# Optimization experiments

Measured on AMD Instinct MI355X. Metric: run time of the kernel, lower is better.

## Reference

```python
import jax, jax.numpy as jnp
import numpy as np

N_NODES = 20000
NUM_KERNELS = 2
K_DIFF = 10  # max_diffusion_step
IN_DIM = 128
HID = 128
COMB = IN_DIM + HID  # 256
N_EDGES = 640000


def setup_inputs() -> dict:
    key = jax.random.key(0)
    ks = jax.random.split(key, 6)
    inp = jax.random.normal(ks[0], (N_NODES, IN_DIM), dtype=jnp.float32)
    hidden = jax.random.normal(ks[1], (N_NODES, HID), dtype=jnp.float32)
    edge_index = jax.random.randint(ks[2], (NUM_KERNELS, 2, N_EDGES), 0, N_NODES, dtype=jnp.int32)
    # ~row-stochastic-ish weights (avg degree 32) to keep diffusion stable
    edge_weight = jax.random.uniform(ks[3], (NUM_KERNELS, N_EDGES), dtype=jnp.float32) * (1.0 / 32.0)
    num_matrices = NUM_KERNELS * K_DIFF + 1  # 21
    W = jax.random.normal(ks[4], (num_matrices * COMB, HID), dtype=jnp.float32) * (1.0 / np.sqrt(num_matrices * COMB))
    b = jnp.zeros((HID,), dtype=jnp.float32)
    return {"input": inp, "hidden": hidden, "edge_index": edge_index,
            "edge_weight": edge_weight, "W": W, "b": b}


def _gconv(x, edge_index, edge_weight, W, b):
    # x: (N, F). Diffusion (Chebyshev) over each sparse support, concat, project.
    n = x.shape[0]
    feats = [x]  # x_0 shared across kernels
    for k in range(NUM_KERNELS):
        src = edge_index[k, 0]
        dst = edge_index[k, 1]
        w = edge_weight[k][:, None]

        def spmm(v):  # (A v)[dst] = sum_e w_e * v[src_e]
            return jax.ops.segment_sum(v[src] * w, dst, num_segments=n)

        x0, x1 = x, spmm(x)
        feats.append(x1)
        for _ in range(2, K_DIFF + 1):
            x2 = 2.0 * spmm(x1) - x0
            feats.append(x2)
            x0, x1 = x1, x2
    h = jnp.concatenate(feats, axis=1)  # (N, (NUM_KERNELS*K+1)*F)
    return h @ W + b


def reference(input, hidden, edge_index, edge_weight, W, b):
    combined = jnp.concatenate([input, hidden], axis=1)  # (N, COMB)
    r = jax.nn.sigmoid(_gconv(combined, edge_index, edge_weight, W, b))
    u = jax.nn.sigmoid(_gconv(combined, edge_index, edge_weight, W, b))
    combined2 = jnp.concatenate([input, r * hidden], axis=1)
    C = jax.nn.sigmoid(_gconv(combined2, edge_index, edge_weight, W, b))  # activation=sigmoid (default)
    output = u * hidden + (1.0 - u) * C
    return output  # output == new hidden
```

## Files before the change

kernel.cpp:

```cpp
#include <hip/hip_runtime.h>

#define NN 20000
#define NK 2
#define FC 256
#define FH 128
#define NE 640000
#define NB 21

typedef short v8s __attribute__((ext_vector_type(8)));
typedef float v4f __attribute__((ext_vector_type(4)));

__device__ __forceinline__ float bf2f(unsigned short h) {
    union { unsigned int u; float f; } v; v.u = ((unsigned int)h) << 16; return v.f;
}
__device__ __forceinline__ unsigned short f2bf(float f) {
    union { float f; unsigned int u; } v; v.f = f;
    unsigned int r = v.u + 0x7FFF + ((v.u >> 16) & 1);
    return (unsigned short)(r >> 16);
}
__device__ __forceinline__ float bflo(unsigned int v) {
    union { unsigned int u; float f; } t; t.u = v << 16; return t.f;
}
__device__ __forceinline__ float bfhi(unsigned int v) {
    union { unsigned int u; float f; } t; t.u = v & 0xffff0000u; return t.f;
}


__global__ __launch_bounds__(256) void k_hist(const int* __restrict__ ei, int* __restrict__ cnt) {
    int i = blockIdx.x * 256 + threadIdx.x;
    int k = i / NE, e = i - k * NE;
    int dst = ei[(size_t)k * 2 * NE + NE + e];
    atomicAdd(&cnt[k * NN + dst], 1);
}

__global__ __launch_bounds__(1024) void k_scan(const int* __restrict__ cnt, int* __restrict__ rp) {
    int k = blockIdx.x;
    __shared__ int part[1024];
    int t = threadIdx.x;
    int loc[20];
    int s = 0;
    if (t < 1000) {
#pragma unroll
        for (int j = 0; j < 20; ++j) { loc[j] = cnt[k * NN + t * 20 + j]; s += loc[j]; }
    }
    part[t] = s;
    __syncthreads();
    for (int off = 1; off < 1024; off <<= 1) {
        int add = (t >= off) ? part[t - off] : 0;
        __syncthreads();
        part[t] += add;
        __syncthreads();
    }
    int excl = (t == 0) ? 0 : part[t - 1];
    if (t < 1000) {
        int run = excl;
#pragma unroll
        for (int j = 0; j < 20; ++j) { rp[k * (NN + 1) + t * 20 + j] = run; run += loc[j]; }
        if (t == 999) rp[k * (NN + 1) + NN] = run;
    }
}

__global__ __launch_bounds__(256) void k_fill(const int* __restrict__ ei, const float* __restrict__ ew,
                                              const int* __restrict__ rp, int* __restrict__ fcnt,
                                              int2* __restrict__ ep) {
    int i = blockIdx.x * 256 + threadIdx.x;
    int k = i / NE, e = i - k * NE;
    int src = ei[(size_t)k * 2 * NE + e];
    int dst = ei[(size_t)k * 2 * NE + NE + e];
    int pos = rp[k * (NN + 1) + dst] + atomicAdd(&fcnt[k * NN + dst], 1);
    int2 pk; pk.x = src; pk.y = __float_as_int(ew[(size_t)k * NE + e]);
    ep[(size_t)k * NE + pos] = pk;
}


__global__ __launch_bounds__(256) void k_comb(const float* __restrict__ in, const float* __restrict__ hid,
                                              unsigned short* __restrict__ comb) {
    int i = blockIdx.x * 256 + threadIdx.x;
    int r = i >> 6, c4 = i & 63;
    float4 v = (c4 < 32) ? ((const float4*)(in  + (size_t)r * FH))[c4]
                         : ((const float4*)(hid + (size_t)r * FH))[c4 - 32];
    ushort4 o; o.x = f2bf(v.x); o.y = f2bf(v.y); o.z = f2bf(v.z); o.w = f2bf(v.w);
    *(ushort4*)&comb[(size_t)r * FC + c4 * 4] = o;
}


__global__ __launch_bounds__(256) void k_wcvt(const float* __restrict__ W, unsigned short* __restrict__ Wt) {
    int i = blockIdx.x * 256 + threadIdx.x;
    int blk = i >> 15;
    int rem = i & 32767;
    int n = rem >> 8, kk = rem & 255;
    Wt[i] = f2bf(W[((size_t)blk * FC + kk) * FH + n]);
}


#define LDK 72

__global__ __launch_bounds__(256, 2) void k_gemm(const unsigned short* __restrict__ X,
        const unsigned short* __restrict__ Wt, unsigned short* __restrict__ outb,
        float* __restrict__ outf, int jstep) {
    __shared__ unsigned short Xs[64 * LDK];
    __shared__ unsigned short Ws[128 * LDK];
    int t = threadIdx.x;
    int w = t >> 6, l = t & 63;
    int l15 = l & 15, lg = l >> 4;
    int bm = blockIdx.x * 64;
    int blk = jstep + 10 * blockIdx.y;
    const unsigned short* Wb = Wt + (size_t)blk * FH * FC;
    v4f acc[4][2];
#pragma unroll
    for (int a = 0; a < 4; ++a)
#pragma unroll
        for (int b = 0; b < 2; ++b) acc[a][b] = (v4f){0.f, 0.f, 0.f, 0.f};

    for (int c = 0; c < 4; ++c) {
#pragma unroll
        for (int i = 0; i < 2; ++i) {
            int s = t + i * 256;
            int row = s >> 3, c8 = s & 7;
            int grow = bm + row; if (grow >= NN) grow = NN - 1;
            *(v8s*)&Xs[row * LDK + c8 * 8] = *(const v8s*)(X + (size_t)grow * FC + c * 64 + c8 * 8);
        }
#pragma unroll
        for (int i = 0; i < 4; ++i) {
            int s = t + i * 256;
            int n = s >> 3, k8 = s & 7;
            *(v8s*)&Ws[n * LDK + k8 * 8] = *(const v8s*)(Wb + (size_t)n * FC + c * 64 + k8 * 8);
        }
        __syncthreads();
#pragma unroll
        for (int ks2 = 0; ks2 < 2; ++ks2) {
            int ko = ks2 * 32 + lg * 8;
            v8s a[4], b[2];
#pragma unroll
            for (int mf = 0; mf < 4; ++mf) a[mf] = *(const v8s*)&Xs[(mf * 16 + l15) * LDK + ko];
#pragma unroll
            for (int nf = 0; nf < 2; ++nf) b[nf] = *(const v8s*)&Ws[(w * 32 + nf * 16 + l15) * LDK + ko];
#pragma unroll
            for (int mf = 0; mf < 4; ++mf)
#pragma unroll
                for (int nf = 0; nf < 2; ++nf)
                    acc[mf][nf] = __builtin_amdgcn_mfma_f32_16x16x32_bf16(a[mf], b[nf], acc[mf][nf], 0, 0, 0);
        }
        __syncthreads();
    }
    unsigned short* ob = outb ? outb + (size_t)blockIdx.y * NN * FH : (unsigned short*)0;
#pragma unroll
    for (int mf = 0; mf < 4; ++mf) {
        int grow0 = bm + mf * 16 + lg * 4;
#pragma unroll
        for (int nf = 0; nf < 2; ++nf) {
            int gcol = w * 32 + nf * 16 + l15;
#pragma unroll
            for (int r = 0; r < 4; ++r) {
                int grow = grow0 + r;
                if (grow < NN) {
                    if (outf) outf[(size_t)grow * FH + gcol] = acc[mf][nf][r];
                    else      ob[(size_t)grow * FH + gcol] = f2bf(acc[mf][nf][r]);
                }
            }
        }
    }
}


__global__ __launch_bounds__(256) void k_spmm(const int* __restrict__ rp, const int2* __restrict__ ep,
        const unsigned short* __restrict__ b1, const unsigned short* __restrict__ b2,
        const unsigned short* __restrict__ y, unsigned short* __restrict__ outp, int mode) {
    int wg = blockIdx.x;
    int xcd = wg & 7, slot = wg >> 3;
    int k = (xcd >= 4) ? 1 : 0;
    int unit = (xcd & 3) * 1250 + slot;
    int lane = threadIdx.x & 63;
    int row = unit * 4 + (threadIdx.x >> 6);
    int beg = rp[k * (NN + 1) + row], end = rp[k * (NN + 1) + row + 1];
    const unsigned int* b1u = (const unsigned int*)b1 + (size_t)k * NN * 64;
    const long long* epk = (const long long*)(ep + (size_t)k * NE);

    float ax0 = 0.f, ax1 = 0.f, ax2 = 0.f, ax3 = 0.f;
    float ay0 = 0.f, ay1 = 0.f, ay2 = 0.f, ay3 = 0.f;

    for (int e0 = beg; e0 < end; e0 += 64) {
        int idx = e0 + lane;
        long long mye = (idx < end) ? __builtin_nontemporal_load(epk + idx) : 0ll;
        int mx = (int)mye;
        int my = (int)(mye >> 32);
        int cnt = min(64, end - e0);
        int j = 0;
        for (; j + 8 <= cnt; j += 8) {
            int   s0 = __builtin_amdgcn_readlane(mx, j + 0);
            int   s1 = __builtin_amdgcn_readlane(mx, j + 1);
            int   s2 = __builtin_amdgcn_readlane(mx, j + 2);
            int   s3 = __builtin_amdgcn_readlane(mx, j + 3);
            int   s4 = __builtin_amdgcn_readlane(mx, j + 4);
            int   s5 = __builtin_amdgcn_readlane(mx, j + 5);
            int   s6 = __builtin_amdgcn_readlane(mx, j + 6);
            int   s7 = __builtin_amdgcn_readlane(mx, j + 7);
            unsigned int v0 = b1u[(size_t)s0 * 64 + lane];
            unsigned int v1 = b1u[(size_t)s1 * 64 + lane];
            unsigned int v2 = b1u[(size_t)s2 * 64 + lane];
            unsigned int v3 = b1u[(size_t)s3 * 64 + lane];
            unsigned int v4 = b1u[(size_t)s4 * 64 + lane];
            unsigned int v5 = b1u[(size_t)s5 * 64 + lane];
            unsigned int v6 = b1u[(size_t)s6 * 64 + lane];
            unsigned int v7 = b1u[(size_t)s7 * 64 + lane];
            float w0 = __int_as_float(__builtin_amdgcn_readlane(my, j + 0));
            float w1 = __int_as_float(__builtin_amdgcn_readlane(my, j + 1));
            float w2 = __int_as_float(__builtin_amdgcn_readlane(my, j + 2));
            float w3 = __int_as_float(__builtin_amdgcn_readlane(my, j + 3));
            float w4 = __int_as_float(__builtin_amdgcn_readlane(my, j + 4));
            float w5 = __int_as_float(__builtin_amdgcn_readlane(my, j + 5));
            float w6 = __int_as_float(__builtin_amdgcn_readlane(my, j + 6));
            float w7 = __int_as_float(__builtin_amdgcn_readlane(my, j + 7));
            ax0 += w0 * bflo(v0); ay0 += w0 * bfhi(v0);
            ax1 += w1 * bflo(v1); ay1 += w1 * bfhi(v1);
            ax2 += w2 * bflo(v2); ay2 += w2 * bfhi(v2);
            ax3 += w3 * bflo(v3); ay3 += w3 * bfhi(v3);
            ax0 += w4 * bflo(v4); ay0 += w4 * bfhi(v4);
            ax1 += w5 * bflo(v5); ay1 += w5 * bfhi(v5);
            ax2 += w6 * bflo(v6); ay2 += w6 * bfhi(v6);
            ax3 += w7 * bflo(v7); ay3 += w7 * bfhi(v7);
        }
        for (; j < cnt; ++j) {
            int   s = __builtin_amdgcn_readlane(mx, j);
            float w = __int_as_float(__builtin_amdgcn_readlane(my, j));
            unsigned int v = b1u[(size_t)s * 64 + lane];
            ax0 += w * bflo(v); ay0 += w * bfhi(v);
        }
    }
    float ax = (ax0 + ax1) + (ax2 + ax3);
    float ay = (ay0 + ay1) + (ay2 + ay3);

    size_t o = (size_t)(k * NN + row) * 64 + lane;
    float rx, ry;
    if (mode == 0) {
        unsigned int yv = __builtin_nontemporal_load((const unsigned int*)y + o);
        rx = bflo(yv) + 2.f * ax;
        ry = bfhi(yv) + 2.f * ay;
    } else if (mode == 1) {
        unsigned int yv = __builtin_nontemporal_load((const unsigned int*)y + o);
        unsigned int bv = __builtin_nontemporal_load((const unsigned int*)b2 + o);
        rx = bflo(yv) + 2.f * ax - bflo(bv);
        ry = bfhi(yv) + 2.f * ay - bfhi(bv);
    } else {
        unsigned int bv = __builtin_nontemporal_load((const unsigned int*)b2 + o);
        rx = ax - bflo(bv);
        ry = ay - bfhi(bv);
    }
    unsigned int res = (unsigned int)f2bf(rx) | ((unsigned int)f2bf(ry) << 16);
    __builtin_nontemporal_store(res, (unsigned int*)outp + o);
}


__global__ __launch_bounds__(256) void k_act(const float* __restrict__ S0, const unsigned short* __restrict__ Sk,
        const float* __restrict__ bvec, const float* __restrict__ hid,
        float* __restrict__ rbuf, unsigned short* __restrict__ comb) {
    int i = blockIdx.x * 256 + threadIdx.x;
    int r = i >> 7, c = i & 127;
    float s = S0[i] + bf2f(Sk[i]) + bf2f(Sk[(size_t)NN * FH + i]) + bvec[c];
    float u = 1.f / (1.f + __expf(-s));
    rbuf[i] = u;
    comb[(size_t)r * FC + FH + c] = f2bf(u * hid[i]);
}

__global__ __launch_bounds__(256) void k_final(const float* __restrict__ S0, const unsigned short* __restrict__ Sk,
        const float* __restrict__ bvec, const float* __restrict__ hid,
        const float* __restrict__ rbuf, float* __restrict__ out) {
    int i = blockIdx.x * 256 + threadIdx.x;
    int c = i & 127;
    float s = S0[i] + bf2f(Sk[i]) + bf2f(Sk[(size_t)NN * FH + i]) + bvec[c];
    float C = 1.f / (1.f + __expf(-s));
    float u = rbuf[i];
    out[i] = u * hid[i] + (1.f - u) * C;
}


extern "C" void kernel_launch(void* const* d_in, const int* in_sizes, int n_in,
                              void* d_out, int out_size, void* d_ws, size_t ws_size,
                              hipStream_t stream) {
    const float* inp = (const float*)d_in[0];
    const float* hid = (const float*)d_in[1];
    const int*   ei  = (const int*)d_in[2];
    const float* ew  = (const float*)d_in[3];
    const float* W   = (const float*)d_in[4];
    const float* bv  = (const float*)d_in[5];
    float* out = (float*)d_out;

    char* base = (char*)d_ws;
    size_t off = 0;
    auto carve = [&](size_t bytes) -> char* {
        char* q = base + off;
        off += (bytes + 255) & ~(size_t)255;
        return q;
    };
    int*            cnt  = (int*)carve((size_t)2 * NN * 4);
    int*            fcnt = (int*)carve((size_t)2 * NN * 4);
    int*            rp   = (int*)carve((size_t)2 * (NN + 1) * 4);
    int2*           ep   = (int2*)carve((size_t)2 * NE * 8);
    unsigned short* comb = (unsigned short*)carve((size_t)NN * FC * 2);
    unsigned short* Wt   = (unsigned short*)carve((size_t)NB * FH * FC * 2);
    unsigned short* ytmp = (unsigned short*)carve((size_t)2 * NN * FH * 2);
    unsigned short* Bs0  = (unsigned short*)carve((size_t)2 * NN * FH * 2);
    unsigned short* Bs1  = (unsigned short*)carve((size_t)2 * NN * FH * 2);
    unsigned short* Bs2  = (unsigned short*)carve((size_t)2 * NN * FH * 2);
    float*          Sacc = (float*)carve((size_t)NN * FH * 4);
    float*          rbuf = (float*)carve((size_t)NN * FH * 4);
    unsigned short* Bsl[3] = {Bs0, Bs1, Bs2};

    hipMemsetAsync(cnt, 0, (size_t)2 * NN * 4, stream);
    hipMemsetAsync(fcnt, 0, (size_t)2 * NN * 4, stream);
    k_hist<<<5000, 256, 0, stream>>>(ei, cnt);
    k_scan<<<2, 1024, 0, stream>>>(cnt, rp);
    k_fill<<<5000, 256, 0, stream>>>(ei, ew, rp, fcnt, ep);
    k_comb<<<5000, 256, 0, stream>>>(inp, hid, comb);
    k_wcvt<<<2688, 256, 0, stream>>>(W, Wt);

    auto gemm = [&](int j, unsigned short* ob, float* of, int gy) {
        k_gemm<<<dim3(313, gy), 256, 0, stream>>>(comb, Wt, ob, of, j);
    };
    auto spmm = [&](unsigned short* b1, unsigned short* b2, unsigned short* y,
                    unsigned short* o, int mode) {
        k_spmm<<<10000, 256, 0, stream>>>(rp, ep, b1, b2, y, o, mode);
    };

    auto gconv = [&]() -> unsigned short* {
        gemm(0, nullptr, Sacc, 1);
        gemm(10, Bsl[0], nullptr, 2);
        gemm(9, ytmp, nullptr, 2);
        spmm(Bsl[0], nullptr, ytmp, Bsl[1], 0);
        int cur = 1, prev = 0;
        for (int j = 8; j >= 1; --j) {
            int nxt = 3 - cur - prev;
            gemm(j, ytmp, nullptr, 2);
            spmm(Bsl[cur], Bsl[prev], ytmp, Bsl[nxt], 1);
            prev = cur; cur = nxt;
        }
        int fr = 3 - cur - prev;
        spmm(Bsl[cur], Bsl[prev], nullptr, Bsl[fr], 2);
        return Bsl[fr];
    };

    unsigned short* S1 = gconv();
    k_act<<<10000, 256, 0, stream>>>(Sacc, S1, bv, hid, rbuf, comb);
    unsigned short* S2 = gconv();
    k_final<<<10000, 256, 0, stream>>>(Sacc, S2, bv, hid, rbuf, out);
}
```

Measured before the change: 1.088 ms.

## Split feature halves across XCDs, batch all projection GEMMs, partition CSR build

Stores the GEMM outputs and diffusion buffers in a half-split layout of 64 columns per half. Each SpMM workgroup, mapped to an XCD, handles one kernel and one half, so the gathered source rows fit better in that XCD's L2. Each wave splits its lanes across two edges and reduces them with a shuffle. When the workspace is large enough, all 21 projection GEMMs run in one launch into a large Y buffer instead of one launch per step. Histogram and fill are partitioned by destination range per XCD, which localizes atomics but makes each edge be read four times.

```diff
diff --git a/kernel.cpp b/kernel.cpp
--- a/kernel.cpp
+++ b/kernel.cpp
@@ -9,28 +9,32 @@
 
 typedef short v8s __attribute__((ext_vector_type(8)));
 typedef float v4f __attribute__((ext_vector_type(4)));
+typedef unsigned int uint;
 
 __device__ __forceinline__ float bf2f(unsigned short h) {
-    union { unsigned int u; float f; } v; v.u = ((unsigned int)h) << 16; return v.f;
+    union { uint u; float f; } v; v.u = ((uint)h) << 16; return v.f;
 }
 __device__ __forceinline__ unsigned short f2bf(float f) {
-    union { float f; unsigned int u; } v; v.f = f;
-    unsigned int r = v.u + 0x7FFF + ((v.u >> 16) & 1);
+    union { float f; uint u; } v; v.f = f;
+    uint r = v.u + 0x7FFF + ((v.u >> 16) & 1);
     return (unsigned short)(r >> 16);
 }
-__device__ __forceinline__ float bflo(unsigned int v) {
-    union { unsigned int u; float f; } t; t.u = v << 16; return t.f;
-}
-__device__ __forceinline__ float bfhi(unsigned int v) {
-    union { unsigned int u; float f; } t; t.u = v & 0xffff0000u; return t.f;
+__device__ __forceinline__ float bflo(uint v) {
+    union { uint u; float f; } t; t.u = v << 16; return t.f;
+}
+__device__ __forceinline__ float bfhi(uint v) {
+    union { uint u; float f; } t; t.u = v & 0xffff0000u; return t.f;
 }
 
 
 __global__ __launch_bounds__(256) void k_hist(const int* __restrict__ ei, int* __restrict__ cnt) {
-    int i = blockIdx.x * 256 + threadIdx.x;
-    int k = i / NE, e = i - k * NE;
+    int wg = blockIdx.x;
+    int xcd = wg & 7, chunk = wg >> 3;
+    int k = xcd & 1, q = xcd >> 1;
+    int e = chunk * 256 + threadIdx.x;
     int dst = ei[(size_t)k * 2 * NE + NE + e];
-    atomicAdd(&cnt[k * NN + dst], 1);
+    if (dst >= q * 5000 && dst < q * 5000 + 5000)
+        atomicAdd(&cnt[k * NN + dst], 1);
 }
 
 __global__ __launch_bounds__(1024) void k_scan(const int* __restrict__ cnt, int* __restrict__ rp) {
@@ -63,13 +67,17 @@
 __global__ __launch_bounds__(256) void k_fill(const int* __restrict__ ei, const float* __restrict__ ew,
                                               const int* __restrict__ rp, int* __restrict__ fcnt,
                                               int2* __restrict__ ep) {
-    int i = blockIdx.x * 256 + threadIdx.x;
-    int k = i / NE, e = i - k * NE;
-    int src = ei[(size_t)k * 2 * NE + e];
+    int wg = blockIdx.x;
+    int xcd = wg & 7, chunk = wg >> 3;
+    int k = xcd & 1, q = xcd >> 1;
+    int e = chunk * 256 + threadIdx.x;
     int dst = ei[(size_t)k * 2 * NE + NE + e];
-    int pos = rp[k * (NN + 1) + dst] + atomicAdd(&fcnt[k * NN + dst], 1);
-    int2 pk; pk.x = src; pk.y = __float_as_int(ew[(size_t)k * NE + e]);
-    ep[(size_t)k * NE + pos] = pk;
+    if (dst >= q * 5000 && dst < q * 5000 + 5000) {
+        int src = ei[(size_t)k * 2 * NE + e];
+        int pos = rp[k * (NN + 1) + dst] + atomicAdd(&fcnt[k * NN + dst], 1);
+        int2 pk; pk.x = src; pk.y = __float_as_int(ew[(size_t)k * NE + e]);
+        ep[(size_t)k * NE + pos] = pk;
+    }
 }
 
 
@@ -97,14 +105,15 @@
 
 __global__ __launch_bounds__(256, 2) void k_gemm(const unsigned short* __restrict__ X,
         const unsigned short* __restrict__ Wt, unsigned short* __restrict__ outb,
-        float* __restrict__ outf, int jstep) {
+        float* __restrict__ outf, int idmode, int blkbase) {
     __shared__ unsigned short Xs[64 * LDK];
     __shared__ unsigned short Ws[128 * LDK];
     int t = threadIdx.x;
     int w = t >> 6, l = t & 63;
     int l15 = l & 15, lg = l >> 4;
     int bm = blockIdx.x * 64;
-    int blk = jstep + 10 * blockIdx.y;
+    int by = blockIdx.y;
+    int blk = idmode ? by : (blkbase + by * 10);
     const unsigned short* Wb = Wt + (size_t)blk * FH * FC;
     v4f acc[4][2];
 #pragma unroll
@@ -143,19 +152,21 @@
         }
         __syncthreads();
     }
-    unsigned short* ob = outb ? outb + (size_t)blockIdx.y * NN * FH : (unsigned short*)0;
+    int isf32 = (idmode && by == 0);
+    unsigned short* ob = outb + (size_t)(by - idmode) * NN * FH;
 #pragma unroll
     for (int mf = 0; mf < 4; ++mf) {
         int grow0 = bm + mf * 16 + lg * 4;
 #pragma unroll
         for (int nf = 0; nf < 2; ++nf) {
             int gcol = w * 32 + nf * 16 + l15;
+            int h = gcol >> 6, c63 = gcol & 63;
 #pragma unroll
             for (int r = 0; r < 4; ++r) {
                 int grow = grow0 + r;
                 if (grow < NN) {
-                    if (outf) outf[(size_t)grow * FH + gcol] = acc[mf][nf][r];
-                    else      ob[(size_t)grow * FH + gcol] = f2bf(acc[mf][nf][r]);
+                    if (isf32) outf[(size_t)grow * FH + gcol] = acc[mf][nf][r];
+                    else       ob[((size_t)h * NN + grow) * 64 + c63] = f2bf(acc[mf][nf][r]);
                 }
             }
         }
@@ -164,16 +175,19 @@
 
 
 __global__ __launch_bounds__(256) void k_spmm(const int* __restrict__ rp, const int2* __restrict__ ep,
-        const unsigned short* __restrict__ b1, const unsigned short* __restrict__ b2,
-        const unsigned short* __restrict__ y, unsigned short* __restrict__ outp, int mode) {
+        const uint* __restrict__ b1u, int b1off, int b1str,
+        const uint* __restrict__ b2u, int b2off, int b2str,
+        const uint* __restrict__ yu, int yoff, int ystr,
+        uint* __restrict__ outu, int mode) {
     int wg = blockIdx.x;
     int xcd = wg & 7, slot = wg >> 3;
-    int k = (xcd >= 4) ? 1 : 0;
-    int unit = (xcd & 3) * 1250 + slot;
+    int c2 = xcd >> 1, hi2 = xcd & 1;
+    int k = c2 >> 1, h = c2 & 1;
+    int row = (hi2 * 2500 + slot) * 4 + (threadIdx.x >> 6);
     int lane = threadIdx.x & 63;
-    int row = unit * 4 + (threadIdx.x >> 6);
+    int l31 = lane & 31, hl = lane >> 5;
     int beg = rp[k * (NN + 1) + row], end = rp[k * (NN + 1) + row + 1];
-    const unsigned int* b1u = (const unsigned int*)b1 + (size_t)k * NN * 64;
+    const uint* __restrict__ gb = b1u + b1off + k * b1str + h * (NN * 32);
     const long long* epk = (const long long*)(ep + (size_t)k * NE);
 
     float ax0 = 0.f, ax1 = 0.f, ax2 = 0.f, ax3 = 0.f;
@@ -187,67 +201,62 @@
         int cnt = min(64, end - e0);
         int j = 0;
         for (; j + 8 <= cnt; j += 8) {
-            int   s0 = __builtin_amdgcn_readlane(mx, j + 0);
-            int   s1 = __builtin_amdgcn_readlane(mx, j + 1);
-            int   s2 = __builtin_amdgcn_readlane(mx, j + 2);
-            int   s3 = __builtin_amdgcn_readlane(mx, j + 3);
-            int   s4 = __builtin_amdgcn_readlane(mx, j + 4);
-            int   s5 = __builtin_amdgcn_readlane(mx, j + 5);
-            int   s6 = __builtin_amdgcn_readlane(mx, j + 6);
-            int   s7 = __builtin_amdgcn_readlane(mx, j + 7);
-            unsigned int v0 = b1u[(size_t)s0 * 64 + lane];
-            unsigned int v1 = b1u[(size_t)s1 * 64 + lane];
-            unsigned int v2 = b1u[(size_t)s2 * 64 + lane];
-            unsigned int v3 = b1u[(size_t)s3 * 64 + lane];
-            unsigned int v4 = b1u[(size_t)s4 * 64 + lane];
-            unsigned int v5 = b1u[(size_t)s5 * 64 + lane];
-            unsigned int v6 = b1u[(size_t)s6 * 64 + lane];
-            unsigned int v7 = b1u[(size_t)s7 * 64 + lane];
-            float w0 = __int_as_float(__builtin_amdgcn_readlane(my, j + 0));
-            float w1 = __int_as_float(__builtin_amdgcn_readlane(my, j + 1));
-            float w2 = __int_as_float(__builtin_amdgcn_readlane(my, j + 2));
-            float w3 = __int_as_float(__builtin_amdgcn_readlane(my, j + 3));
-            float w4 = __int_as_float(__builtin_amdgcn_readlane(my, j + 4));
-            float w5 = __int_as_float(__builtin_amdgcn_readlane(my, j + 5));
-            float w6 = __int_as_float(__builtin_amdgcn_readlane(my, j + 6));
-            float w7 = __int_as_float(__builtin_amdgcn_readlane(my, j + 7));
+            int p0 = j + hl, p1 = j + 2 + hl, p2 = j + 4 + hl, p3 = j + 6 + hl;
+            int s0 = __shfl(mx, p0), s1 = __shfl(mx, p1), s2 = __shfl(mx, p2), s3 = __shfl(mx, p3);
+            uint v0 = gb[(uint)(s0 * 32 + l31)];
+            uint v1 = gb[(uint)(s1 * 32 + l31)];
+            uint v2 = gb[(uint)(s2 * 32 + l31)];
+            uint v3 = gb[(uint)(s3 * 32 + l31)];
+            float w0 = __int_as_float(__shfl(my, p0));
+            float w1 = __int_as_float(__shfl(my, p1));
+            float w2 = __int_as_float(__shfl(my, p2));
+            float w3 = __int_as_float(__shfl(my, p3));
             ax0 += w0 * bflo(v0); ay0 += w0 * bfhi(v0);
             ax1 += w1 * bflo(v1); ay1 += w1 * bfhi(v1);
             ax2 += w2 * bflo(v2); ay2 += w2 * bfhi(v2);
             ax3 += w3 * bflo(v3); ay3 += w3 * bfhi(v3);
-            ax0 += w4 * bflo(v4); ay0 += w4 * bfhi(v4);
-            ax1 += w5 * bflo(v5); ay1 += w5 * bfhi(v5);
-            ax2 += w6 * bflo(v6); ay2 += w6 * bfhi(v6);
-            ax3 += w7 * bflo(v7); ay3 += w7 * bfhi(v7);
-        }
-        for (; j < cnt; ++j) {
-            int   s = __builtin_amdgcn_readlane(mx, j);
-            float w = __int_as_float(__builtin_amdgcn_readlane(my, j));
-            unsigned int v = b1u[(size_t)s * 64 + lane];
+        }
+        for (; j + 2 <= cnt; j += 2) {
+            int p = j + hl;
+            int s = __shfl(mx, p);
+            uint v = gb[(uint)(s * 32 + l31)];
+            float w = __int_as_float(__shfl(my, p));
             ax0 += w * bflo(v); ay0 += w * bfhi(v);
+        }
+        if (j < cnt) {
+            int s = __shfl(mx, j);
+            float w = __int_as_float(__shfl(my, j));
+            if (hl == 0) {
+                uint v = gb[(uint)(s * 32 + l31)];
+                ax0 += w * bflo(v); ay0 += w * bfhi(v);
+            }
         }
     }
     float ax = (ax0 + ax1) + (ax2 + ax3);
     float ay = (ay0 + ay1) + (ay2 + ay3);
-
-    size_t o = (size_t)(k * NN + row) * 64 + lane;
-    float rx, ry;
-    if (mode == 0) {
-        unsigned int yv = __builtin_nontemporal_load((const unsigned int*)y + o);
-        rx = bflo(yv) + 2.f * ax;
-        ry = bfhi(yv) + 2.f * ay;
-    } else if (mode == 1) {
-        unsigned int yv = __builtin_nontemporal_load((const unsigned int*)y + o);
-        unsigned int bv = __builtin_nontemporal_load((const unsigned int*)b2 + o);
-        rx = bflo(yv) + 2.f * ax - bflo(bv);
-        ry = bfhi(yv) + 2.f * ay - bfhi(bv);
-    } else {
-        unsigned int bv = __builtin_nontemporal_load((const unsigned int*)b2 + o);
-        rx = ax - bflo(bv);
-        ry = ay - bfhi(bv);
-    }
-    unsigned int res = (unsigned int)f2bf(rx) | ((unsigned int)f2bf(ry) << 16);
-    __builtin_nontemporal_store(res, (unsigned int*)outp + o);
+    ax += __shfl_xor(ax, 32);
+    ay += __shfl_xor(ay, 32);
+
+    if (hl == 0) {
+        int o_out = k * (NN * 64) + (h * NN + row) * 32 + l31;
+        float rx, ry;
+        if (mode == 0) {
+            uint yv = __builtin_nontemporal_load(yu + yoff + k * ystr + (h * NN + row) * 32 + l31);
+            rx = bflo(yv) + 2.f * ax;
+            ry = bfhi(yv) + 2.f * ay;
+        } else if (mode == 1) {
+            uint yv = __builtin_nontemporal_load(yu + yoff + k * ystr + (h * NN + row) * 32 + l31);
+            uint bv = __builtin_nontemporal_load(b2u + b2off + k * b2str + (h * NN + row) * 32 + l31);
+            rx = bflo(yv) + 2.f * ax - bflo(bv);
+            ry = bfhi(yv) + 2.f * ay - bfhi(bv);
+        } else {
+            uint bv = __builtin_nontemporal_load(b2u + b2off + k * b2str + (h * NN + row) * 32 + l31);
+            rx = ax - bflo(bv);
+            ry = ay - bfhi(bv);
+        }
+        uint res = (uint)f2bf(rx) | ((uint)f2bf(ry) << 16);
+        __builtin_nontemporal_store(res, outu + o_out);
+    }
 }
 
 
@@ -256,7 +265,9 @@
         float* __restrict__ rbuf, unsigned short* __restrict__ comb) {
     int i = blockIdx.x * 256 + threadIdx.x;
     int r = i >> 7, c = i & 127;
-    float s = S0[i] + bf2f(Sk[i]) + bf2f(Sk[(size_t)NN * FH + i]) + bvec[c];
+    int h = c >> 6, c63 = c & 63;
+    float s = S0[i] + bf2f(Sk[((size_t)h * NN + r) * 64 + c63])
+                    + bf2f(Sk[((size_t)(2 + h) * NN + r) * 64 + c63]) + bvec[c];
     float u = 1.f / (1.f + __expf(-s));
     rbuf[i] = u;
     comb[(size_t)r * FC + FH + c] = f2bf(u * hid[i]);
@@ -266,8 +277,10 @@
         const float* __restrict__ bvec, const float* __restrict__ hid,
         const float* __restrict__ rbuf, float* __restrict__ out) {
     int i = blockIdx.x * 256 + threadIdx.x;
-    int c = i & 127;
-    float s = S0[i] + bf2f(Sk[i]) + bf2f(Sk[(size_t)NN * FH + i]) + bvec[c];
+    int r = i >> 7, c = i & 127;
+    int h = c >> 6, c63 = c & 63;
+    float s = S0[i] + bf2f(Sk[((size_t)h * NN + r) * 64 + c63])
+                    + bf2f(Sk[((size_t)(2 + h) * NN + r) * 64 + c63]) + bvec[c];
     float C = 1.f / (1.f + __expf(-s));
     float u = rbuf[i];
     out[i] = u * hid[i] + (1.f - u) * C;
@@ -292,50 +305,81 @@
         off += (bytes + 255) & ~(size_t)255;
         return q;
     };
-    int*            cnt  = (int*)carve((size_t)2 * NN * 4);
-    int*            fcnt = (int*)carve((size_t)2 * NN * 4);
-    int*            rp   = (int*)carve((size_t)2 * (NN + 1) * 4);
-    int2*           ep   = (int2*)carve((size_t)2 * NE * 8);
-    unsigned short* comb = (unsigned short*)carve((size_t)NN * FC * 2);
-    unsigned short* Wt   = (unsigned short*)carve((size_t)NB * FH * FC * 2);
-    unsigned short* ytmp = (unsigned short*)carve((size_t)2 * NN * FH * 2);
-    unsigned short* Bs0  = (unsigned short*)carve((size_t)2 * NN * FH * 2);
-    unsigned short* Bs1  = (unsigned short*)carve((size_t)2 * NN * FH * 2);
-    unsigned short* Bs2  = (unsigned short*)carve((size_t)2 * NN * FH * 2);
-    float*          Sacc = (float*)carve((size_t)NN * FH * 4);
-    float*          rbuf = (float*)carve((size_t)NN * FH * 4);
+    int*            cnt   = (int*)carve((size_t)2 * NN * 4);
+    int*            fcnt  = (int*)carve((size_t)2 * NN * 4);
+    int*            rp    = (int*)carve((size_t)2 * (NN + 1) * 4);
+    int2*           ep    = (int2*)carve((size_t)2 * NE * 8);
+    unsigned short* comb  = (unsigned short*)carve((size_t)NN * FC * 2);
+    unsigned short* Wt    = (unsigned short*)carve((size_t)NB * FH * FC * 2);
+    unsigned short* ytA   = (unsigned short*)carve((size_t)2 * NN * FH * 2);
+    unsigned short* ytB   = (unsigned short*)carve((size_t)2 * NN * FH * 2);
+    unsigned short* Bs0   = (unsigned short*)carve((size_t)2 * NN * FH * 2);
+    unsigned short* Bs1   = (unsigned short*)carve((size_t)2 * NN * FH * 2);
+    unsigned short* Bs2   = (unsigned short*)carve((size_t)2 * NN * FH * 2);
+    float*          Sacc  = (float*)carve((size_t)NN * FH * 4);
+    float*          rbuf  = (float*)carve((size_t)NN * FH * 4);
+    size_t yall_bytes = (size_t)20 * NN * FH * 2;
+    int use_big = (off + yall_bytes + 256 <= ws_size);
+    unsigned short* Yall = use_big ? (unsigned short*)carve(yall_bytes) : (unsigned short*)0;
     unsigned short* Bsl[3] = {Bs0, Bs1, Bs2};
+
+    const int BSTR = NN * 64;
+    const int YSTR = 10 * NN * 64;
 
     hipMemsetAsync(cnt, 0, (size_t)2 * NN * 4, stream);
     hipMemsetAsync(fcnt, 0, (size_t)2 * NN * 4, stream);
-    k_hist<<<5000, 256, 0, stream>>>(ei, cnt);
+    k_hist<<<20000, 256, 0, stream>>>(ei, cnt);
     k_scan<<<2, 1024, 0, stream>>>(cnt, rp);
-    k_fill<<<5000, 256, 0, stream>>>(ei, ew, rp, fcnt, ep);
+    k_fill<<<20000, 256, 0, stream>>>(ei, ew, rp, fcnt, ep);
     k_comb<<<5000, 256, 0, stream>>>(inp, hid, comb);
     k_wcvt<<<2688, 256, 0, stream>>>(W, Wt);
 
-    auto gemm = [&](int j, unsigned short* ob, float* of, int gy) {
-        k_gemm<<<dim3(313, gy), 256, 0, stream>>>(comb, Wt, ob, of, j);
+    auto spmm = [&](const unsigned short* b1, int b1off, int b1str,
+                    const unsigned short* b2, int b2off, int b2str,
+                    const unsigned short* y, int yoff, int ystr,
+                    unsigned short* o, int mode) {
+        k_spmm<<<20000, 256, 0, stream>>>(rp, ep,
+            (const uint*)b1, b1off, b1str, (const uint*)b2, b2off, b2str,
+            (const uint*)y, yoff, ystr, (uint*)o, mode);
     };
-    auto spmm = [&](unsigned short* b1, unsigned short* b2, unsigned short* y,
-                    unsigned short* o, int mode) {
-        k_spmm<<<10000, 256, 0, stream>>>(rp, ep, b1, b2, y, o, mode);
-    };
 
     auto gconv = [&]() -> unsigned short* {
-        gemm(0, nullptr, Sacc, 1);
-        gemm(10, Bsl[0], nullptr, 2);
-        gemm(9, ytmp, nullptr, 2);
-        spmm(Bsl[0], nullptr, ytmp, Bsl[1], 0);
-        int cur = 1, prev = 0;
+        int cur, prev;
+        int jstart;
+        const unsigned short* b10p; int b10off, b10str;
+        if (use_big) {
+            k_gemm<<<dim3(313, 21), 256, 0, stream>>>(comb, Wt, Yall, Sacc, 1, 0);
+            spmm(Yall, 9 * NN * 64, YSTR, nullptr, 0, 0, Yall, 8 * NN * 64, YSTR, Bsl[0], 0);
+            b10p = Yall; b10off = 9 * NN * 64; b10str = YSTR;
+        } else {
+            k_gemm<<<dim3(313, 1), 256, 0, stream>>>(comb, Wt, ytA, Sacc, 1, 0);
+            k_gemm<<<dim3(313, 2), 256, 0, stream>>>(comb, Wt, ytA, Sacc, 0, 10);
+            k_gemm<<<dim3(313, 2), 256, 0, stream>>>(comb, Wt, ytB, Sacc, 0, 9);
+            spmm(ytA, 0, BSTR, nullptr, 0, 0, ytB, 0, BSTR, Bsl[0], 0);
+            b10p = ytA; b10off = 0; b10str = BSTR;
+        }
+        cur = 0; prev = -1;
         for (int j = 8; j >= 1; --j) {
-            int nxt = 3 - cur - prev;
-            gemm(j, ytmp, nullptr, 2);
-            spmm(Bsl[cur], Bsl[prev], ytmp, Bsl[nxt], 1);
+            int nxt;
+            const unsigned short* yp; int yo, ys;
+            if (use_big) {
+                yp = Yall; yo = (j - 1) * NN * 64; ys = YSTR;
+            } else {
+                unsigned short* tb = (((8 - j) & 1) == 0) ? ytB : ytA;
+                k_gemm<<<dim3(313, 2), 256, 0, stream>>>(comb, Wt, tb, Sacc, 0, j);
+                yp = tb; yo = 0; ys = BSTR;
+            }
+            if (prev < 0) {
+                nxt = 1;
+                spmm(Bsl[cur], 0, BSTR, b10p, b10off, b10str, yp, yo, ys, Bsl[nxt], 1);
+            } else {
+                nxt = 3 - cur - prev;
+                spmm(Bsl[cur], 0, BSTR, Bsl[prev], 0, BSTR, yp, yo, ys, Bsl[nxt], 1);
+            }
             prev = cur; cur = nxt;
         }
         int fr = 3 - cur - prev;
-        spmm(Bsl[cur], Bsl[prev], nullptr, Bsl[fr], 2);
+        spmm(Bsl[cur], 0, BSTR, Bsl[prev], 0, BSTR, nullptr, 0, 0, Bsl[fr], 2);
         return Bsl[fr];
     };
 
```

Result: slower. 1.292 ms (+18.7%).
